# Kernel optimization log

Measured on AMD Instinct MI355X. Metric: run time of the kernel, lower is better.

Reference implementation:

```python
import jax, jax.numpy as jnp
import numpy as np

D_MODEL = 1024
N_HEAD = 16
D_HEAD = D_MODEL // N_HEAD


def setup_inputs() -> dict:
    key = jax.random.key(0)
    k_x, k_qkv, k_proj = jax.random.split(key, 3)
    B, T = 2, 2048
    x = jax.random.normal(k_x, (B, T, D_MODEL), dtype=jnp.float32)
    # torch Linear weight [out, in]; y = x @ W.T. Scale ~ kaiming-uniform-ish.
    s = 1.0 / np.sqrt(D_MODEL)
    W_qkv = jax.random.uniform(k_qkv, (3 * D_MODEL, D_MODEL), dtype=jnp.float32, minval=-s, maxval=s)
    W_proj = jax.random.uniform(k_proj, (D_MODEL, D_MODEL), dtype=jnp.float32, minval=-s, maxval=s)
    return {"x": x, "W_qkv": W_qkv, "W_proj": W_proj}


def reference(x, W_qkv, W_proj):
    B, T, C = x.shape
    qkv = jnp.einsum('btc,oc->bto', x, W_qkv)  # [B,T,3C]
    q, k, v = jnp.split(qkv, 3, axis=-1)
    # [B,T,C] -> [B,H,T,Dh]
    def heads(t):
        return t.reshape(B, T, N_HEAD, D_HEAD).transpose(0, 2, 1, 3)
    q, k, v = heads(q), heads(k), heads(v)
    scale = 1.0 / np.sqrt(D_HEAD)
    scores = jnp.einsum('bhqd,bhkd->bhqk', q, k) * scale  # [B,H,T,T]
    causal = jnp.tril(jnp.ones((T, T), dtype=bool))
    scores = jnp.where(causal, scores, jnp.finfo(scores.dtype).min)
    attn = jax.nn.softmax(scores, axis=-1)
    y = jnp.einsum('bhqk,bhkd->bhqd', attn, v)  # [B,H,T,Dh]
    y = y.transpose(0, 2, 1, 3).reshape(B, T, C)
    return jnp.einsum('btc,oc->bto', y, W_proj)
```

## Files before the change

### kernel.cpp

```cpp
#include <hip/hip_runtime.h>

typedef unsigned short u16;
typedef float f32x4 __attribute__((ext_vector_type(4)));
typedef __bf16 bf16x8 __attribute__((ext_vector_type(8)));
typedef unsigned int u32x4 __attribute__((ext_vector_type(4)));
typedef u16 u16x4 __attribute__((ext_vector_type(4)));
typedef u16 u16x8 __attribute__((ext_vector_type(8)));

static __device__ __forceinline__ u16 f2bf(float f) {
  union { __bf16 h; u16 u; } c;
  c.h = (__bf16)f;
  return c.u;
}

static __device__ __forceinline__ void gload_lds16(const void* g, void* l) {
  __builtin_amdgcn_global_load_lds(
      (const __attribute__((address_space(1))) unsigned int*)g,
      (__attribute__((address_space(3))) unsigned int*)l, 16, 0, 0);
}

__global__ __launch_bounds__(256) void cvt_f32_bf16(const float* __restrict__ in,
                                                    u16* __restrict__ out, int n4) {
  int i = blockIdx.x * 256 + threadIdx.x;
  if (i < n4) {
    f32x4 v = *((const f32x4*)in + i);
    u16x4 o;
    o[0] = f2bf(v[0]); o[1] = f2bf(v[1]); o[2] = f2bf(v[2]); o[3] = f2bf(v[3]);
    *((u16x4*)out + i) = o;
  }
}

template<int OUT_BF16>
__global__ __launch_bounds__(256) void gemm_nt(const u16* __restrict__ A,
                                               const u16* __restrict__ B,
                                               void* __restrict__ Cp,
                                               int M, int N, int K) {
  __shared__ __align__(16) u16 lA[128 * 64];
  __shared__ __align__(16) u16 lB[128 * 64];
  const int tid = threadIdx.x;
  const int lane = tid & 63;
  const int wave = tid >> 6;
  const int wm = wave >> 1, wn = wave & 1;
  const int l15 = lane & 15, lg = lane >> 4;
  const int bm = blockIdx.y * 128, bn = blockIdx.x * 128;

  f32x4 acc[4][4];
#pragma unroll
  for (int i = 0; i < 4; ++i)
#pragma unroll
    for (int j = 0; j < 4; ++j) acc[i][j] = (f32x4){0.f, 0.f, 0.f, 0.f};

  const u16* Ag[4];
  const u16* Bg[4];
#pragma unroll
  for (int it = 0; it < 4; ++it) {
    const int s = it * 256 + tid;
    const int row = s >> 3, g = s & 7;
    const int gsw = g ^ (row & 7);
    Ag[it] = A + (size_t)(bm + row) * K + gsw * 8;
    Bg[it] = B + (size_t)(bn + row) * K + gsw * 8;
  }

  for (int k0 = 0; k0 < K; k0 += 64) {
#pragma unroll
    for (int it = 0; it < 4; ++it) {
      gload_lds16(Ag[it] + k0, (u16*)lA + (size_t)(it * 256 + tid) * 8);
      gload_lds16(Bg[it] + k0, (u16*)lB + (size_t)(it * 256 + tid) * 8);
    }
    __syncthreads();
#pragma unroll
    for (int kk = 0; kk < 2; ++kk) {
      bf16x8 af[4], bfv[4];
#pragma unroll
      for (int mf = 0; mf < 4; ++mf) {
        const int row = wm * 64 + mf * 16 + l15;
        af[mf] = *(const bf16x8*)((const char*)lA + row * 128 +
                                  ((kk * 64 + lg * 16) ^ ((row & 7) << 4)));
      }
#pragma unroll
      for (int nf = 0; nf < 4; ++nf) {
        const int row = wn * 64 + nf * 16 + l15;
        bfv[nf] = *(const bf16x8*)((const char*)lB + row * 128 +
                                   ((kk * 64 + lg * 16) ^ ((row & 7) << 4)));
      }
#pragma unroll
      for (int mf = 0; mf < 4; ++mf)
#pragma unroll
        for (int nf = 0; nf < 4; ++nf)
          acc[mf][nf] = __builtin_amdgcn_mfma_f32_16x16x32_bf16(af[mf], bfv[nf], acc[mf][nf], 0, 0, 0);
    }
    __syncthreads();
  }

#pragma unroll
  for (int mf = 0; mf < 4; ++mf) {
#pragma unroll
    for (int r = 0; r < 4; ++r) {
      const int row = bm + wm * 64 + mf * 16 + lg * 4 + r;
#pragma unroll
      for (int nf = 0; nf < 4; ++nf) {
        const int col = bn + wn * 64 + nf * 16 + l15;
        const float v = acc[mf][nf][r];
        if (OUT_BF16) ((u16*)Cp)[(size_t)row * N + col] = f2bf(v);
        else          ((float*)Cp)[(size_t)row * N + col] = v;
      }
    }
  }
}

__global__ __launch_bounds__(256) void transpose_v(const u16* __restrict__ qkv,
                                                   u16* __restrict__ vt) {
  constexpr int T = 2048, C3 = 3072, D = 64;
  __shared__ u16 lt[64 * 65];
  const int t0 = blockIdx.x * 64;
  const int bh = blockIdx.y;
  const int b = bh >> 4, h = bh & 15;
  const int tid = threadIdx.x;
#pragma unroll
  for (int it = 0; it < 2; ++it) {
    const int c = tid + it * 256;
    const int tr = c >> 3, d0 = (c & 7) * 8;
    u32x4 v = *(const u32x4*)&qkv[((size_t)b * T + t0 + tr) * C3 + 2048 + h * D + d0];
    const u16* pv = (const u16*)&v;
#pragma unroll
    for (int e = 0; e < 8; ++e) lt[tr * 65 + d0 + e] = pv[e];
  }
  __syncthreads();
#pragma unroll
  for (int it = 0; it < 2; ++it) {
    const int c = tid + it * 256;
    const int d = c >> 3, toff = (c & 7) * 8;
    u16x8 tmp;
#pragma unroll
    for (int e = 0; e < 8; ++e) tmp[e] = lt[(toff + e) * 65 + d];
    *(u16x8*)&vt[((size_t)bh * D + d) * T + t0 + toff] = tmp;
  }
}

__global__ __launch_bounds__(256) void attn_fwd(const u16* __restrict__ qkv,
                                                const u16* __restrict__ vt,
                                                u16* __restrict__ y) {
  constexpr int T = 2048, C = 1024, C3 = 3072, D = 64, NQ = 32;
  __shared__ __align__(16) u16 lK[2][64 * 64];
  __shared__ __align__(16) u16 lV[2][64 * 64];
  __shared__ __align__(16) u16 lP[4 * 16 * 64];
  const int tid = threadIdx.x, lane = tid & 63, w = tid >> 6;
  const int l15 = lane & 15, lg = lane >> 4;

  const int bid = blockIdx.x;
  const int xcd = bid & 7, slot = bid >> 3;
  const int bh = xcd * 4 + (slot >> 4);
  const int pi = slot & 15;
  const int b = bh >> 4, h = bh & 15;

  const int r0 = tid >> 3, off0 = (tid & 7) * 8;
  const int r1 = (tid + 256) >> 3, off1 = off0;
  const int sb0 = (off0 * 2) ^ ((r0 & 7) << 4);
  const int sb1 = (off1 * 2) ^ ((r1 & 7) << 4);
  const u16* Kbase = qkv + (size_t)b * T * C3 + C + h * D;
  const u16* Vbase = vt + (size_t)bh * D * T;

  const float qscale = 0.125f * 1.44269504088896f;

#pragma unroll 1
  for (int qi = 0; qi < 2; ++qi) {
    const int qt = (qi == 0) ? pi : (NQ - 1 - pi);
    const int q0 = qt * 64;

    const size_t qoff = ((size_t)b * T + q0 + w * 16 + l15) * C3 + h * D;
    const bf16x8 aq0 = *(const bf16x8*)&qkv[qoff + lg * 8];
    const bf16x8 aq1 = *(const bf16x8*)&qkv[qoff + 32 + lg * 8];

    float m_r[4], l_r[4];
    f32x4 o_acc[4];
#pragma unroll
    for (int r = 0; r < 4; ++r) { m_r[r] = -1.0e30f; l_r[r] = 0.f; }
#pragma unroll
    for (int nf = 0; nf < 4; ++nf) o_acc[nf] = (f32x4){0.f, 0.f, 0.f, 0.f};

    u32x4 rk0 = *(const u32x4*)(Kbase + (size_t)r0 * C3 + off0);
    u32x4 rk1 = *(const u32x4*)(Kbase + (size_t)r1 * C3 + off1);
    u32x4 rv0 = *(const u32x4*)(Vbase + (size_t)r0 * T + off0);
    u32x4 rv1 = *(const u32x4*)(Vbase + (size_t)r1 * T + off1);
    __syncthreads();
    *(u32x4*)&lK[0][(r0 * 128 + sb0) >> 1] = rk0;
    *(u32x4*)&lK[0][(r1 * 128 + sb1) >> 1] = rk1;
    *(u32x4*)&lV[0][(r0 * 128 + sb0) >> 1] = rv0;
    *(u32x4*)&lV[0][(r1 * 128 + sb1) >> 1] = rv1;
    if (qt > 0) {
      rk0 = *(const u32x4*)(Kbase + (size_t)(64 + r0) * C3 + off0);
      rk1 = *(const u32x4*)(Kbase + (size_t)(64 + r1) * C3 + off1);
      rv0 = *(const u32x4*)(Vbase + (size_t)r0 * T + 64 + off0);
      rv1 = *(const u32x4*)(Vbase + (size_t)r1 * T + 64 + off1);
    }

    for (int kt = 0; kt <= qt; ++kt) {
      const int cur = kt & 1;
      __syncthreads();
      if (kt < qt) {
        *(u32x4*)&lK[cur ^ 1][(r0 * 128 + sb0) >> 1] = rk0;
        *(u32x4*)&lK[cur ^ 1][(r1 * 128 + sb1) >> 1] = rk1;
        *(u32x4*)&lV[cur ^ 1][(r0 * 128 + sb0) >> 1] = rv0;
        *(u32x4*)&lV[cur ^ 1][(r1 * 128 + sb1) >> 1] = rv1;
        if (kt + 1 < qt) {
          const int kn = (kt + 2) * 64;
          rk0 = *(const u32x4*)(Kbase + (size_t)(kn + r0) * C3 + off0);
          rk1 = *(const u32x4*)(Kbase + (size_t)(kn + r1) * C3 + off1);
          rv0 = *(const u32x4*)(Vbase + (size_t)r0 * T + kn + off0);
          rv1 = *(const u32x4*)(Vbase + (size_t)r1 * T + kn + off1);
        }
      }
      const u16* Kc = lK[cur];
      const u16* Vc = lV[cur];

      f32x4 s[4];
#pragma unroll
      for (int nf = 0; nf < 4; ++nf) s[nf] = (f32x4){0.f, 0.f, 0.f, 0.f};
      __builtin_amdgcn_s_setprio(1);
#pragma unroll
      for (int nf = 0; nf < 4; ++nf) {
        const int row = nf * 16 + l15;
        const int x = (row & 7) << 4;
        bf16x8 bk0 = *(const bf16x8*)&Kc[(row * 128 + ((lg * 16) ^ x)) >> 1];
        bf16x8 bk1 = *(const bf16x8*)&Kc[(row * 128 + ((64 + lg * 16) ^ x)) >> 1];
        s[nf] = __builtin_amdgcn_mfma_f32_16x16x32_bf16(aq0, bk0, s[nf], 0, 0, 0);
        s[nf] = __builtin_amdgcn_mfma_f32_16x16x32_bf16(aq1, bk1, s[nf], 0, 0, 0);
      }
      __builtin_amdgcn_s_setprio(0);

#pragma unroll
      for (int nf = 0; nf < 4; ++nf) {
#pragma unroll
        for (int r = 0; r < 4; ++r) {
          float v = s[nf][r] * qscale;
          if (kt == qt) {
            if (nf * 16 + l15 > w * 16 + lg * 4 + r) v = -1.0e30f;
          }
          s[nf][r] = v;
        }
      }

      float p[4][4];
#pragma unroll
      for (int r = 0; r < 4; ++r) {
        float mx = fmaxf(fmaxf(s[0][r], s[1][r]), fmaxf(s[2][r], s[3][r]));
        mx = fmaxf(mx, __shfl_xor(mx, 1));
        mx = fmaxf(mx, __shfl_xor(mx, 2));
        mx = fmaxf(mx, __shfl_xor(mx, 4));
        mx = fmaxf(mx, __shfl_xor(mx, 8));
        const float mnew = fmaxf(m_r[r], mx);
        const float fct = __builtin_amdgcn_exp2f(m_r[r] - mnew);
        float sum = 0.f;
#pragma unroll
        for (int nf = 0; nf < 4; ++nf) {
          const float pv = __builtin_amdgcn_exp2f(s[nf][r] - mnew);
          p[nf][r] = pv;
          sum += pv;
        }
        sum += __shfl_xor(sum, 1);
        sum += __shfl_xor(sum, 2);
        sum += __shfl_xor(sum, 4);
        sum += __shfl_xor(sum, 8);
        l_r[r] = l_r[r] * fct + sum;
        m_r[r] = mnew;
#pragma unroll
        for (int nf = 0; nf < 4; ++nf) o_acc[nf][r] *= fct;
      }

#pragma unroll
      for (int r = 0; r < 4; ++r) {
        const int i = lg * 4 + r;
#pragma unroll
        for (int nf = 0; nf < 4; ++nf) {
          const int j = nf * 16 + l15;
          lP[(w * 2048 + i * 128 + ((j * 2) ^ ((i & 7) << 4))) >> 1] = f2bf(p[nf][r]);
        }
      }

      __builtin_amdgcn_s_setprio(1);
#pragma unroll
      for (int sj = 0; sj < 2; ++sj) {
        bf16x8 ap = *(const bf16x8*)&lP[(w * 2048 + l15 * 128 + ((sj * 64 + lg * 16) ^ ((l15 & 7) << 4))) >> 1];
#pragma unroll
        for (int nf = 0; nf < 4; ++nf) {
          const int d = nf * 16 + l15;
          bf16x8 bv = *(const bf16x8*)&Vc[(d * 128 + ((sj * 64 + lg * 16) ^ ((d & 7) << 4))) >> 1];
          o_acc[nf] = __builtin_amdgcn_mfma_f32_16x16x32_bf16(ap, bv, o_acc[nf], 0, 0, 0);
        }
      }
      __builtin_amdgcn_s_setprio(0);
    }

#pragma unroll
    for (int nf = 0; nf < 4; ++nf) {
#pragma unroll
      for (int r = 0; r < 4; ++r) {
        const int row = q0 + w * 16 + lg * 4 + r;
        const int col = h * D + nf * 16 + l15;
        y[((size_t)b * T + row) * C + col] = f2bf(o_acc[nf][r] / l_r[r]);
      }
    }
  }
}

extern "C" void kernel_launch(void* const* d_in, const int* in_sizes, int n_in,
                              void* d_out, int out_size, void* d_ws, size_t ws_size,
                              hipStream_t stream) {
  const float* x = (const float*)d_in[0];
  const float* Wqkv = (const float*)d_in[1];
  const float* Wproj = (const float*)d_in[2];
  float* out = (float*)d_out;

  constexpr int B = 2, T = 2048, C = 1024, C3 = 3072, H = 16, D = 64;
  constexpr int M = B * T;

  u16* xb = (u16*)d_ws;
  u16* wqkvb = xb + (size_t)M * C;
  u16* wprojb = wqkvb + (size_t)C3 * C;
  u16* qkvb = wprojb + (size_t)C * C;
  u16* vtb = qkvb + (size_t)M * C3;
  u16* yb = vtb + (size_t)M * C;

  cvt_f32_bf16<<<dim3((M * C) / 4 / 256), 256, 0, stream>>>(x, xb, (M * C) / 4);
  cvt_f32_bf16<<<dim3((C3 * C) / 4 / 256), 256, 0, stream>>>(Wqkv, wqkvb, (C3 * C) / 4);
  cvt_f32_bf16<<<dim3((C * C) / 4 / 256), 256, 0, stream>>>(Wproj, wprojb, (C * C) / 4);

  gemm_nt<1><<<dim3(C3 / 128, M / 128), 256, 0, stream>>>(xb, wqkvb, qkvb, M, C3, C);
  transpose_v<<<dim3(T / 64, B * H), 256, 0, stream>>>(qkvb, vtb);
  attn_fwd<<<dim3(512), 256, 0, stream>>>(qkvb, vtb, yb);
  gemm_nt<0><<<dim3(C / 128, M / 128), 256, 0, stream>>>(yb, wprojb, out, M, C, C);
}
```

Before: 136.1 us.

## Transpose QK^T MFMA so each lane owns one query row in softmax

Swaps the MFMA operand order so the score tile is transposed, giving each lane a single query row (indexed by l15) whose keys sit in registers. Row max and sum now need only two cross-lane shuffles instead of four per row, with one scalar m and l per lane. The P tile is written to LDS as packed 4-element vectors. The output rescale is skipped when no lane's max grows, and the final divide becomes a reciprocal multiply. The cost is extra shuffles to broadcast the rescale factor and l back to the accumulator layout, a wave-wide vote branch, and a slightly less exact reciprocal.

Measured after the change: 118.5 us. 12.9% less time.

```diff
diff --git a/kernel.cpp b/kernel.cpp
--- a/kernel.cpp
+++ b/kernel.cpp
@@ -171,10 +171,8 @@
     const bf16x8 aq0 = *(const bf16x8*)&qkv[qoff + lg * 8];
     const bf16x8 aq1 = *(const bf16x8*)&qkv[qoff + 32 + lg * 8];
 
-    float m_r[4], l_r[4];
+    float m = -1.0e30f, l = 0.f;
     f32x4 o_acc[4];
-#pragma unroll
-    for (int r = 0; r < 4; ++r) { m_r[r] = -1.0e30f; l_r[r] = 0.f; }
 #pragma unroll
     for (int nf = 0; nf < 4; ++nf) o_acc[nf] = (f32x4){0.f, 0.f, 0.f, 0.f};
 
@@ -223,8 +221,8 @@
         const int x = (row & 7) << 4;
         bf16x8 bk0 = *(const bf16x8*)&Kc[(row * 128 + ((lg * 16) ^ x)) >> 1];
         bf16x8 bk1 = *(const bf16x8*)&Kc[(row * 128 + ((64 + lg * 16) ^ x)) >> 1];
-        s[nf] = __builtin_amdgcn_mfma_f32_16x16x32_bf16(aq0, bk0, s[nf], 0, 0, 0);
-        s[nf] = __builtin_amdgcn_mfma_f32_16x16x32_bf16(aq1, bk1, s[nf], 0, 0, 0);
+        s[nf] = __builtin_amdgcn_mfma_f32_16x16x32_bf16(bk0, aq0, s[nf], 0, 0, 0);
+        s[nf] = __builtin_amdgcn_mfma_f32_16x16x32_bf16(bk1, aq1, s[nf], 0, 0, 0);
       }
       __builtin_amdgcn_s_setprio(0);
 
@@ -234,47 +232,53 @@
         for (int r = 0; r < 4; ++r) {
           float v = s[nf][r] * qscale;
           if (kt == qt) {
-            if (nf * 16 + l15 > w * 16 + lg * 4 + r) v = -1.0e30f;
+            if (nf * 16 + lg * 4 + r > w * 16 + l15) v = -1.0e30f;
           }
           s[nf][r] = v;
         }
       }
 
+      float t0a = fmaxf(fmaxf(s[0][0], s[0][1]), fmaxf(s[0][2], s[0][3]));
+      float t1a = fmaxf(fmaxf(s[1][0], s[1][1]), fmaxf(s[1][2], s[1][3]));
+      float t2a = fmaxf(fmaxf(s[2][0], s[2][1]), fmaxf(s[2][2], s[2][3]));
+      float t3a = fmaxf(fmaxf(s[3][0], s[3][1]), fmaxf(s[3][2], s[3][3]));
+      float pmax = fmaxf(fmaxf(t0a, t1a), fmaxf(t2a, t3a));
+      pmax = fmaxf(pmax, __shfl_xor(pmax, 16));
+      pmax = fmaxf(pmax, __shfl_xor(pmax, 32));
+
+      if (!__all(pmax <= m)) {
+        const float mnew = fmaxf(m, pmax);
+        const float fct = __builtin_amdgcn_exp2f(m - mnew);
+        m = mnew;
+        l *= fct;
+#pragma unroll
+        for (int r = 0; r < 4; ++r) {
+          const float fr = __shfl(fct, lg * 4 + r);
+#pragma unroll
+          for (int nf = 0; nf < 4; ++nf) o_acc[nf][r] *= fr;
+        }
+      }
+
       float p[4][4];
 #pragma unroll
-      for (int r = 0; r < 4; ++r) {
-        float mx = fmaxf(fmaxf(s[0][r], s[1][r]), fmaxf(s[2][r], s[3][r]));
-        mx = fmaxf(mx, __shfl_xor(mx, 1));
-        mx = fmaxf(mx, __shfl_xor(mx, 2));
-        mx = fmaxf(mx, __shfl_xor(mx, 4));
-        mx = fmaxf(mx, __shfl_xor(mx, 8));
-        const float mnew = fmaxf(m_r[r], mx);
-        const float fct = __builtin_amdgcn_exp2f(m_r[r] - mnew);
-        float sum = 0.f;
-#pragma unroll
-        for (int nf = 0; nf < 4; ++nf) {
-          const float pv = __builtin_amdgcn_exp2f(s[nf][r] - mnew);
-          p[nf][r] = pv;
-          sum += pv;
-        }
-        sum += __shfl_xor(sum, 1);
-        sum += __shfl_xor(sum, 2);
-        sum += __shfl_xor(sum, 4);
-        sum += __shfl_xor(sum, 8);
-        l_r[r] = l_r[r] * fct + sum;
-        m_r[r] = mnew;
-#pragma unroll
-        for (int nf = 0; nf < 4; ++nf) o_acc[nf][r] *= fct;
-      }
-
-#pragma unroll
-      for (int r = 0; r < 4; ++r) {
-        const int i = lg * 4 + r;
-#pragma unroll
-        for (int nf = 0; nf < 4; ++nf) {
-          const int j = nf * 16 + l15;
-          lP[(w * 2048 + i * 128 + ((j * 2) ^ ((i & 7) << 4))) >> 1] = f2bf(p[nf][r]);
-        }
+      for (int nf = 0; nf < 4; ++nf)
+#pragma unroll
+        for (int r = 0; r < 4; ++r) p[nf][r] = __builtin_amdgcn_exp2f(s[nf][r] - m);
+      float s0a = (p[0][0] + p[0][1]) + (p[0][2] + p[0][3]);
+      float s1a = (p[1][0] + p[1][1]) + (p[1][2] + p[1][3]);
+      float s2a = (p[2][0] + p[2][1]) + (p[2][2] + p[2][3]);
+      float s3a = (p[3][0] + p[3][1]) + (p[3][2] + p[3][3]);
+      float psum = (s0a + s1a) + (s2a + s3a);
+      psum += __shfl_xor(psum, 16);
+      psum += __shfl_xor(psum, 32);
+      l += psum;
+
+#pragma unroll
+      for (int nf = 0; nf < 4; ++nf) {
+        u16x4 pk;
+        pk[0] = f2bf(p[nf][0]); pk[1] = f2bf(p[nf][1]);
+        pk[2] = f2bf(p[nf][2]); pk[3] = f2bf(p[nf][3]);
+        *(u16x4*)&lP[(w * 2048 + l15 * 128 + ((nf * 32 + lg * 8) ^ ((l15 & 7) << 4))) >> 1] = pk;
       }
 
       __builtin_amdgcn_s_setprio(1);
@@ -292,12 +296,13 @@
     }
 
 #pragma unroll
-    for (int nf = 0; nf < 4; ++nf) {
-#pragma unroll
-      for (int r = 0; r < 4; ++r) {
-        const int row = q0 + w * 16 + lg * 4 + r;
+    for (int r = 0; r < 4; ++r) {
+      const float li = __builtin_amdgcn_rcpf(__shfl(l, lg * 4 + r));
+      const int row = q0 + w * 16 + lg * 4 + r;
+#pragma unroll
+      for (int nf = 0; nf < 4; ++nf) {
         const int col = h * D + nf * 16 + l15;
-        y[((size_t)b * T + row) * C + col] = f2bf(o_acc[nf][r] / l_r[r]);
+        y[((size_t)b * T + row) * C + col] = f2bf(o_acc[nf][r] * li);
       }
     }
   }
```
